# Kernel optimization log

Measured on AMD Instinct MI355X. Metric: run time of the kernel, lower is better.

Reference implementation:

```python
import jax, jax.numpy as jnp
import numpy as np

NUM_CLUSTERS = 256
MAX_ITERS = 10
TOL = 1e-4
N, D = 262144, 64


def setup_inputs() -> dict:
    key = jax.random.key(0)
    k_data, k_perm = jax.random.split(key)
    data = jax.random.normal(k_data, (N, D), dtype=jnp.float32)
    # torch.randperm(len(data))[:num_clusters] -> distinct init indices
    init_indices = jax.random.permutation(k_perm, N)[:NUM_CLUSTERS].astype(jnp.int64)
    return {"data": data, "init_indices": init_indices}


def _sq_dists(x, c):
    x2 = jnp.sum(x * x, axis=1, keepdims=True)        # [N, 1]
    c2 = jnp.sum(c * c, axis=1)[None, :]              # [1, K]
    return x2 + c2 - 2.0 * (x @ c.T)                  # [N, K]


def reference(data, init_indices):
    centroids0 = data[init_indices]                    # [K, D]
    labels0 = jnp.zeros(data.shape[0], dtype=jnp.int32)
    ones = jnp.ones((data.shape[0],), dtype=data.dtype)

    def step(carry, _):
        centroids, labels, done = carry
        d2 = _sq_dists(data, centroids)
        new_labels = jnp.where(done, labels, jnp.argmin(d2, axis=1).astype(jnp.int32))
        # single-pass segment mean (torch: stack of masked means; empty -> nan, matched by 0/0)
        sums = jax.ops.segment_sum(data, new_labels, num_segments=NUM_CLUSTERS)
        counts = jax.ops.segment_sum(ones, new_labels, num_segments=NUM_CLUSTERS)
        new_centroids = sums / counts[:, None]
        delta = jnp.linalg.norm(new_centroids - centroids)
        new_done = done | (delta < TOL)
        centroids = jnp.where(done, centroids, new_centroids)
        return (centroids, new_labels, new_done), None

    (_, labels, _), _ = jax.lax.scan(
        step, (centroids0, labels0, jnp.array(False)), None, length=MAX_ITERS
    )
    return labels
```

## Files before the change

### kernel.cpp

```cpp
#include <hip/hip_runtime.h>
#include <math.h>

#define N_PTS 262144
#define KC 256
#define DIM 64
#define MAX_ITERS 10
#define CHUNK 256


__device__ __forceinline__ float seq_rowsum_sq64(const float* p)
{
    float s = fmaf(p[0], p[0], 0.f);
    #pragma unroll
    for (int d = 1; d < DIM; ++d) s = s + fmaf(p[d], p[d], 0.f);
    return s;
}

__global__ void detect_idx(const int* __restrict__ a, int* __restrict__ mode)
{
    int zeros = 0;
    for (int j = 1; j < 256; j += 2) zeros += (a[j] == 0);
    *mode = (zeros >= 2) ? 1 : 0;
}

__global__ __launch_bounds__(256) void init_gather(
    const float* __restrict__ data, const void* __restrict__ idxraw,
    const int* __restrict__ mode,
    float* __restrict__ C, int* __restrict__ done)
{
    int t = blockIdx.x * 256 + threadIdx.x;
    if (t < KC * DIM) {
        int k = t >> 6;
        long long src = (*mode) ? ((const long long*)idxraw)[k]
                                : (long long)((const int*)idxraw)[k];
        C[t] = data[(size_t)src * DIM + (t & 63)];
    }
    if (t == 0) *done = 0;
}

__global__ __launch_bounds__(256) void c2_init(
    const float* __restrict__ C, float* __restrict__ c2, int* __restrict__ nanidx)
{
    int k = threadIdx.x;
    float p[DIM];
    #pragma unroll
    for (int d = 0; d < DIM; ++d) p[d] = C[k * DIM + d];
    c2[k] = seq_rowsum_sq64(p);
    __syncthreads();
    if (k == 0) {
        int ni = -1;
        for (int kk = 0; kk < KC; ++kk)
            if (isnan(c2[kk])) { ni = kk; break; }
        *nanidx = ni;
    }
}

__global__ __launch_bounds__(256) void assign_k(
    const float* __restrict__ data, const float* __restrict__ C,
    const float* __restrict__ c2, const int* __restrict__ nanidx,
    int* __restrict__ labels, const int* __restrict__ done)
{
    if (*done) return;
    int i = blockIdx.x * 256 + threadIdx.x;
    int ni = *nanidx;
    if (ni >= 0) { labels[i] = ni; return; }

    float p[DIM];
    const float4* r = (const float4*)(data + (size_t)i * DIM);
    #pragma unroll
    for (int j = 0; j < 16; ++j) {
        float4 v = r[j];
        p[4 * j + 0] = v.x; p[4 * j + 1] = v.y;
        p[4 * j + 2] = v.z; p[4 * j + 3] = v.w;
    }
    float xx = seq_rowsum_sq64(p);

    float bestd = INFINITY;
    int best = 0;
    for (int k0 = 0; k0 < KC; k0 += 4) {
        const float* c0 = C + (size_t)k0 * DIM;
        float a0 = 0.f, a1 = 0.f, a2 = 0.f, a3 = 0.f;
        #pragma unroll
        for (int d = 0; d < DIM; ++d) {
            float pd = p[d];
            a0 = fmaf(c0[d], pd, a0);
            a1 = fmaf(c0[DIM + d], pd, a1);
            a2 = fmaf(c0[2 * DIM + d], pd, a2);
            a3 = fmaf(c0[3 * DIM + d], pd, a3);
        }
        float d0 = (xx + c2[k0 + 0]) - 2.f * a0;
        float d1 = (xx + c2[k0 + 1]) - 2.f * a1;
        float d2v = (xx + c2[k0 + 2]) - 2.f * a2;
        float d3 = (xx + c2[k0 + 3]) - 2.f * a3;
        if (d0 < bestd) { bestd = d0; best = k0 + 0; }
        if (d1 < bestd) { bestd = d1; best = k0 + 1; }
        if (d2v < bestd) { bestd = d2v; best = k0 + 2; }
        if (d3 < bestd) { bestd = d3; best = k0 + 3; }
    }
    labels[i] = best;
}

__global__ __launch_bounds__(256) void hist_k(
    const int* __restrict__ labels, int* __restrict__ hist,
    const int* __restrict__ done)
{
    if (*done) return;
    __shared__ int h[KC];
    int b = blockIdx.x;
    h[threadIdx.x] = 0;
    __syncthreads();
    int base = b * 1024;
    for (int j = threadIdx.x; j < 1024; j += 256)
        atomicAdd(&h[labels[base + j]], 1);
    __syncthreads();
    hist[b * KC + threadIdx.x] = h[threadIdx.x];
}

__global__ __launch_bounds__(256) void prefix_k(
    int* __restrict__ hist, int* __restrict__ seg_start,
    float* __restrict__ counts, const int* __restrict__ done)
{
    if (*done) return;
    int k = threadIdx.x;
    int run = 0;
    #pragma unroll 8
    for (int b = 0; b < 256; ++b) {
        int v = hist[b * KC + k];
        hist[b * KC + k] = run;
        run += v;
    }
    __shared__ int sc[KC];
    sc[k] = run;
    __syncthreads();
    for (int off = 1; off < KC; off <<= 1) {
        int v = (k >= off) ? sc[k - off] : 0;
        __syncthreads();
        sc[k] += v;
        __syncthreads();
    }
    int base = sc[k] - run;
    seg_start[k] = base;
    if (k == 0) seg_start[KC] = N_PTS;
    counts[k] = (float)run;
    #pragma unroll 8
    for (int b = 0; b < 256; ++b)
        hist[b * KC + k] += base;
}

__global__ __launch_bounds__(256) void scatter_k(
    const int* __restrict__ labels, const int* __restrict__ hist,
    int* __restrict__ order, const int* __restrict__ done)
{
    if (*done) return;
    __shared__ int lab_s[1024];
    int b = blockIdx.x, k = threadIdx.x;
    int base = b * 1024;
    for (int j = k; j < 1024; j += 256) lab_s[j] = labels[base + j];
    __syncthreads();
    int pos = hist[b * KC + k];
    for (int j = 0; j < 1024; ++j) {
        if (lab_s[j] == k) order[pos++] = base + j;
    }
}

__global__ __launch_bounds__(512, 1) void sum_pipe4(
    const float* __restrict__ data, const int* __restrict__ order,
    const int* __restrict__ seg_start, float* __restrict__ sums,
    const int* __restrict__ done)
{
    if (*done) return;
    __shared__ float buf[2][DIM][CHUNK];
    int k = blockIdx.x;
    int t = threadIdx.x;
    int beg = seg_start[k], end = seg_start[k + 1];
    int n = end - beg;
    int nchunk = (n + CHUNK - 1) / CHUNK;
    bool stager = (t >= 64);
    int st = t - 64;

    int gg[3], qq[3];
    #pragma unroll
    for (int i = 0; i < 3; ++i) {
        int G = st + i * 448;
        gg[i] = G >> 4;
        qq[i] = G & 15;
    }
    int ordA[12];
    const float4* d4 = (const float4*)data;

#define ORDX(cc)                                                              \
    {                                                                         \
        int _b = beg + (cc) * CHUNK;                                          \
        int _m = n - (cc) * CHUNK; if (_m > CHUNK) _m = CHUNK;                \
        _Pragma("unroll")                                                     \
        for (int i = 0; i < 3; ++i) {                                         \
            _Pragma("unroll")                                                 \
            for (int r = 0; r < 4; ++r) {                                     \
                int _rr = 4 * gg[i] + r; if (_rr >= _m) _rr = _m - 1;         \
                ordA[i * 4 + r] = order[_b + _rr];                            \
            }                                                                 \
        }                                                                     \
    }
#define STAGEX(cc, which)                                                     \
    {                                                                         \
        int _m = n - (cc) * CHUNK; if (_m > CHUNK) _m = CHUNK;                \
        int _ng = (_m + 3) >> 2;                                              \
        float4* _bp = (float4*)&buf[which][0][0];                             \
        _Pragma("unroll")                                                     \
        for (int i = 0; i < 3; ++i) {                                         \
            if (gg[i] < _ng) {                                                \
                float4 a0 = d4[(size_t)ordA[i * 4 + 0] * 16 + qq[i]];         \
                float4 a1 = d4[(size_t)ordA[i * 4 + 1] * 16 + qq[i]];         \
                float4 a2 = d4[(size_t)ordA[i * 4 + 2] * 16 + qq[i]];         \
                float4 a3 = d4[(size_t)ordA[i * 4 + 3] * 16 + qq[i]];         \
                int _d0 = qq[i] * 4;                                          \
                _bp[(_d0 + 0) * (CHUNK / 4) + (gg[i] ^ ((_d0 + 0) & 7))] =    \
                    make_float4(a0.x, a1.x, a2.x, a3.x);                      \
                _bp[(_d0 + 1) * (CHUNK / 4) + (gg[i] ^ ((_d0 + 1) & 7))] =    \
                    make_float4(a0.y, a1.y, a2.y, a3.y);                      \
                _bp[(_d0 + 2) * (CHUNK / 4) + (gg[i] ^ ((_d0 + 2) & 7))] =    \
                    make_float4(a0.z, a1.z, a2.z, a3.z);                      \
                _bp[(_d0 + 3) * (CHUNK / 4) + (gg[i] ^ ((_d0 + 3) & 7))] =    \
                    make_float4(a0.w, a1.w, a2.w, a3.w);                      \
            }                                                                 \
        }                                                                     \
    }

    if (stager && nchunk > 0) {
        ORDX(0);
        STAGEX(0, 0);
        if (nchunk > 1) ORDX(1);
    }
    __syncthreads();

    float s = 0.f;
    int x7 = t & 7;
    for (int c = 0; c < nchunk; ++c) {
        if (stager) {
            if (c + 1 < nchunk) STAGEX(c + 1, (c + 1) & 1);
            if (c + 2 < nchunk) ORDX(c + 2);
        } else {
            int m = n - c * CHUNK; if (m > CHUNK) m = CHUNK;
            int mg = m >> 2;
            int cur = c & 1;
            const float4* rp = (const float4*)&buf[cur][t][0];
            #pragma unroll 8
            for (int g = 0; g < mg; ++g) {
                float4 v = rp[g ^ x7];
                s = s + v.x; s = s + v.y; s = s + v.z; s = s + v.w;
            }
            for (int j = mg * 4; j < m; ++j)
                s = s + buf[cur][t][(((j >> 2) ^ x7) << 2) + (j & 3)];
        }
        __syncthreads();
    }
#undef ORDX
#undef STAGEX
    if (t < 64) sums[k * DIM + t] = s;
}

__global__ __launch_bounds__(64) void accum_scan(
    const float* __restrict__ data, const int* __restrict__ labels,
    float* __restrict__ sums, float* __restrict__ counts,
    const int* __restrict__ done)
{
    if (*done) return;
    int k = blockIdx.x;
    int d = threadIdx.x;
    __shared__ int lab_s[1024];
    float s = 0.f;
    int cnt = 0;
    for (int base = 0; base < N_PTS; base += 1024) {
        for (int j = d; j < 1024; j += 64) lab_s[j] = labels[base + j];
        __syncthreads();
        #pragma unroll 8
        for (int j = 0; j < 1024; ++j) {
            if (lab_s[j] == k) { s = s + data[(size_t)(base + j) * DIM + d]; ++cnt; }
        }
        __syncthreads();
    }
    sums[k * DIM + d] = s;
    if (d == 0) counts[k] = (float)cnt;
}

__global__ __launch_bounds__(256) void update_c2_k(
    float* __restrict__ C, const float* __restrict__ sums,
    const float* __restrict__ counts, float* __restrict__ c2,
    int* __restrict__ nanidx, int* __restrict__ done)
{
    if (*done) return;
    __shared__ double red[256];
    int k = threadIdx.x;

    float cnt = counts[k];
    float nc[DIM];
    double local = 0.0;
    #pragma unroll
    for (int d = 0; d < DIM; ++d) {
        float v = sums[k * DIM + d] / cnt;
        nc[d] = v;
        float old = C[k * DIM + d];
        double diff = (double)v - (double)old;
        local = fma(diff, diff, local);
        C[k * DIM + d] = v;
    }
    c2[k] = seq_rowsum_sq64(nc);

    red[k] = local;
    __syncthreads();
    if (k == 0) {
        int ni = -1;
        for (int kk = 0; kk < KC; ++kk)
            if (isnan(c2[kk])) { ni = kk; break; }
        *nanidx = ni;
    }
    for (int s = 128; s > 0; s >>= 1) {
        if (k < s) red[k] += red[k + s];
        __syncthreads();
    }
    if (k == 0 && red[0] < 1e-8) *done = 1;
}

extern "C" void kernel_launch(void* const* d_in, const int* in_sizes, int n_in,
                              void* d_out, int out_size, void* d_ws, size_t ws_size,
                              hipStream_t stream)
{
    const float* data = (const float*)d_in[0];
    const void*  idx  = d_in[1];
    int* labels = (int*)d_out;

    float* C      = (float*)d_ws;
    float* sums   = C + KC * DIM;
    float* counts = sums + KC * DIM;
    float* c2     = counts + KC;
    int*   done      = (int*)(c2 + KC);
    int*   mode      = done + 1;
    int*   nanidx    = done + 2;
    int*   seg_start = done + 4;
    int*   hist      = seg_start + 260;
    int*   order     = hist + KC * 256;
    size_t need_sort = (size_t)((char*)(order + N_PTS) - (char*)d_ws);
    bool fast = ws_size >= need_sort;

    detect_idx<<<1, 1, 0, stream>>>((const int*)idx, mode);
    init_gather<<<64, 256, 0, stream>>>(data, idx, mode, C, done);
    c2_init<<<1, 256, 0, stream>>>(C, c2, nanidx);

    for (int it = 0; it < MAX_ITERS; ++it) {
        assign_k<<<N_PTS / 256, 256, 0, stream>>>(data, C, c2, nanidx, labels, done);
        if (fast) {
            hist_k<<<256, 256, 0, stream>>>(labels, hist, done);
            prefix_k<<<1, 256, 0, stream>>>(hist, seg_start, counts, done);
            scatter_k<<<256, 256, 0, stream>>>(labels, hist, order, done);
            sum_pipe4<<<KC, 512, 0, stream>>>(data, order, seg_start, sums, done);
        } else {
            accum_scan<<<KC, 64, 0, stream>>>(data, labels, sums, counts, done);
        }
        update_c2_k<<<1, 256, 0, stream>>>(C, sums, counts, c2, nanidx, done);
    }
}
```

Measured before the change: 3.099 ms.

## Stage centroids in shared memory and compute two points per thread in assign

The assignment kernel now copies the whole 64KB centroid table into LDS once per block and reads it as float4 broadcasts. Each thread handles two points, so every centroid load feeds twice as many FMAs, and the grid is halved. This removes repeated global or scalar-cache centroid reads and raises arithmetic intensity. In exchange the kernel needs 64KB of LDS per block, which caps blocks per CU, and it doubles register use for the two 64-float point rows.

```diff
diff --git a/kernel.cpp b/kernel.cpp
--- a/kernel.cpp
+++ b/kernel.cpp
@@ -55,49 +55,94 @@
     }
 }
 
-__global__ __launch_bounds__(256) void assign_k(
-    const float* __restrict__ data, const float* __restrict__ C,
+__global__ __launch_bounds__(256, 2) void assign_k(
+    const float* __restrict__ data, const float* __restrict__ Cin,
     const float* __restrict__ c2, const int* __restrict__ nanidx,
     int* __restrict__ labels, const int* __restrict__ done)
 {
     if (*done) return;
-    int i = blockIdx.x * 256 + threadIdx.x;
+    __shared__ float Cs[KC * DIM];
+    int i0 = blockIdx.x * 256 + threadIdx.x;
+    int i1 = i0 + N_PTS / 2;
     int ni = *nanidx;
-    if (ni >= 0) { labels[i] = ni; return; }
-
-    float p[DIM];
-    const float4* r = (const float4*)(data + (size_t)i * DIM);
-    #pragma unroll
-    for (int j = 0; j < 16; ++j) {
-        float4 v = r[j];
-        p[4 * j + 0] = v.x; p[4 * j + 1] = v.y;
-        p[4 * j + 2] = v.z; p[4 * j + 3] = v.w;
-    }
-    float xx = seq_rowsum_sq64(p);
-
-    float bestd = INFINITY;
-    int best = 0;
+    if (ni >= 0) { labels[i0] = ni; labels[i1] = ni; return; }
+
+    {
+        const float4* cg = (const float4*)Cin;
+        float4* cs = (float4*)Cs;
+        #pragma unroll
+        for (int j = 0; j < 16; ++j)
+            cs[threadIdx.x + j * 256] = cg[threadIdx.x + j * 256];
+    }
+    __syncthreads();
+
+    float p0[DIM], p1[DIM];
+    {
+        const float4* r0 = (const float4*)(data + (size_t)i0 * DIM);
+        const float4* r1 = (const float4*)(data + (size_t)i1 * DIM);
+        #pragma unroll
+        for (int j = 0; j < 16; ++j) {
+            float4 v0 = r0[j], v1 = r1[j];
+            p0[4 * j + 0] = v0.x; p0[4 * j + 1] = v0.y;
+            p0[4 * j + 2] = v0.z; p0[4 * j + 3] = v0.w;
+            p1[4 * j + 0] = v1.x; p1[4 * j + 1] = v1.y;
+            p1[4 * j + 2] = v1.z; p1[4 * j + 3] = v1.w;
+        }
+    }
+    float xx0 = seq_rowsum_sq64(p0);
+    float xx1 = seq_rowsum_sq64(p1);
+
+    float bd0 = INFINITY, bd1 = INFINITY;
+    int bk0 = 0, bk1 = 0;
     for (int k0 = 0; k0 < KC; k0 += 4) {
-        const float* c0 = C + (size_t)k0 * DIM;
-        float a0 = 0.f, a1 = 0.f, a2 = 0.f, a3 = 0.f;
+        const float4* c0 = (const float4*)(Cs + (size_t)k0 * DIM);
+        float a00 = 0.f, a01 = 0.f, a02 = 0.f, a03 = 0.f;
+        float a10 = 0.f, a11 = 0.f, a12 = 0.f, a13 = 0.f;
         #pragma unroll
-        for (int d = 0; d < DIM; ++d) {
-            float pd = p[d];
-            a0 = fmaf(c0[d], pd, a0);
-            a1 = fmaf(c0[DIM + d], pd, a1);
-            a2 = fmaf(c0[2 * DIM + d], pd, a2);
-            a3 = fmaf(c0[3 * DIM + d], pd, a3);
+        for (int dq = 0; dq < 16; ++dq) {
+            float4 c_0 = c0[dq];
+            float4 c_1 = c0[16 + dq];
+            float4 c_2 = c0[32 + dq];
+            float4 c_3 = c0[48 + dq];
+            int d = dq * 4;
+            a00 = fmaf(c_0.x, p0[d + 0], a00); a00 = fmaf(c_0.y, p0[d + 1], a00);
+            a00 = fmaf(c_0.z, p0[d + 2], a00); a00 = fmaf(c_0.w, p0[d + 3], a00);
+            a01 = fmaf(c_1.x, p0[d + 0], a01); a01 = fmaf(c_1.y, p0[d + 1], a01);
+            a01 = fmaf(c_1.z, p0[d + 2], a01); a01 = fmaf(c_1.w, p0[d + 3], a01);
+            a02 = fmaf(c_2.x, p0[d + 0], a02); a02 = fmaf(c_2.y, p0[d + 1], a02);
+            a02 = fmaf(c_2.z, p0[d + 2], a02); a02 = fmaf(c_2.w, p0[d + 3], a02);
+            a03 = fmaf(c_3.x, p0[d + 0], a03); a03 = fmaf(c_3.y, p0[d + 1], a03);
+            a03 = fmaf(c_3.z, p0[d + 2], a03); a03 = fmaf(c_3.w, p0[d + 3], a03);
+            a10 = fmaf(c_0.x, p1[d + 0], a10); a10 = fmaf(c_0.y, p1[d + 1], a10);
+            a10 = fmaf(c_0.z, p1[d + 2], a10); a10 = fmaf(c_0.w, p1[d + 3], a10);
+            a11 = fmaf(c_1.x, p1[d + 0], a11); a11 = fmaf(c_1.y, p1[d + 1], a11);
+            a11 = fmaf(c_1.z, p1[d + 2], a11); a11 = fmaf(c_1.w, p1[d + 3], a11);
+            a12 = fmaf(c_2.x, p1[d + 0], a12); a12 = fmaf(c_2.y, p1[d + 1], a12);
+            a12 = fmaf(c_2.z, p1[d + 2], a12); a12 = fmaf(c_2.w, p1[d + 3], a12);
+            a13 = fmaf(c_3.x, p1[d + 0], a13); a13 = fmaf(c_3.y, p1[d + 1], a13);
+            a13 = fmaf(c_3.z, p1[d + 2], a13); a13 = fmaf(c_3.w, p1[d + 3], a13);
         }
-        float d0 = (xx + c2[k0 + 0]) - 2.f * a0;
-        float d1 = (xx + c2[k0 + 1]) - 2.f * a1;
-        float d2v = (xx + c2[k0 + 2]) - 2.f * a2;
-        float d3 = (xx + c2[k0 + 3]) - 2.f * a3;
-        if (d0 < bestd) { bestd = d0; best = k0 + 0; }
-        if (d1 < bestd) { bestd = d1; best = k0 + 1; }
-        if (d2v < bestd) { bestd = d2v; best = k0 + 2; }
-        if (d3 < bestd) { bestd = d3; best = k0 + 3; }
-    }
-    labels[i] = best;
+        float c2_0 = c2[k0 + 0], c2_1 = c2[k0 + 1];
+        float c2_2 = c2[k0 + 2], c2_3 = c2[k0 + 3];
+        float e00 = (xx0 + c2_0) - 2.f * a00;
+        float e01 = (xx0 + c2_1) - 2.f * a01;
+        float e02 = (xx0 + c2_2) - 2.f * a02;
+        float e03 = (xx0 + c2_3) - 2.f * a03;
+        float e10 = (xx1 + c2_0) - 2.f * a10;
+        float e11 = (xx1 + c2_1) - 2.f * a11;
+        float e12 = (xx1 + c2_2) - 2.f * a12;
+        float e13 = (xx1 + c2_3) - 2.f * a13;
+        if (e00 < bd0) { bd0 = e00; bk0 = k0 + 0; }
+        if (e01 < bd0) { bd0 = e01; bk0 = k0 + 1; }
+        if (e02 < bd0) { bd0 = e02; bk0 = k0 + 2; }
+        if (e03 < bd0) { bd0 = e03; bk0 = k0 + 3; }
+        if (e10 < bd1) { bd1 = e10; bk1 = k0 + 0; }
+        if (e11 < bd1) { bd1 = e11; bk1 = k0 + 1; }
+        if (e12 < bd1) { bd1 = e12; bk1 = k0 + 2; }
+        if (e13 < bd1) { bd1 = e13; bk1 = k0 + 3; }
+    }
+    labels[i0] = bk0;
+    labels[i1] = bk1;
 }
 
 __global__ __launch_bounds__(256) void hist_k(
@@ -347,7 +392,7 @@
     c2_init<<<1, 256, 0, stream>>>(C, c2, nanidx);
 
     for (int it = 0; it < MAX_ITERS; ++it) {
-        assign_k<<<N_PTS / 256, 256, 0, stream>>>(data, C, c2, nanidx, labels, done);
+        assign_k<<<N_PTS / 512, 256, 0, stream>>>(data, C, c2, nanidx, labels, done);
         if (fast) {
             hist_k<<<256, 256, 0, stream>>>(labels, hist, done);
             prefix_k<<<1, 256, 0, stream>>>(hist, seg_start, counts, done);
```

After: 2.687 ms. 1.15x faster.
